# Kernel optimization log

Measured on AMD Instinct MI355X. Metric: run time of the kernel, lower is better.

## Reference

```python
import jax, jax.numpy as jnp
import numpy as np

WS = 8   # window_size
NH = 4   # num_heads
EPS = 1e-5

def _rel_pos_index(ws):
    # Static Swin relative-position index, computed with numpy (constant).
    coords = np.stack(np.meshgrid(np.arange(ws), np.arange(ws), indexing='ij'))  # [2,ws,ws]
    cf = coords.reshape(2, -1)                       # [2, N]
    rel = cf[:, :, None] - cf[:, None, :]            # [2, N, N]
    rel = rel.transpose(1, 2, 0).copy()              # [N, N, 2]
    rel[:, :, 0] += ws - 1
    rel[:, :, 1] += ws - 1
    rel[:, :, 0] *= 2 * ws - 1
    return jnp.asarray(rel.sum(-1))                  # [N, N] int

def setup_inputs() -> dict:
    key = jax.random.key(0)
    ks = jax.random.split(key, 4)
    B, C, H, W = 8, 64, 256, 256
    return {
        'x': jax.random.normal(ks[0], (B, C, H, W), jnp.float32),
        'norm_w': jnp.ones((C,), jnp.float32),
        'norm_b': jnp.zeros((C,), jnp.float32),
        'qkv_w': jax.random.normal(ks[1], (3 * C, C), jnp.float32) * 0.05,
        'proj_w': jax.random.normal(ks[2], (C, C), jnp.float32) * 0.05,
        'attn_scale': jnp.ones((1,), jnp.float32) * 0.2,
        'rpb_table': jax.random.normal(ks[3], ((2 * WS - 1) ** 2, NH), jnp.float32) * 0.02,
    }

def reference(x, norm_w, norm_b, qkv_w, proj_w, attn_scale, rpb_table):
    B, C, H, W = x.shape
    ws, nh = WS, NH
    hd = C // nh
    N = ws * ws
    nwh, nww = H // ws, W // ws  # H,W multiples of ws -> pad branch is a no-op
    # window partition: [B,C,H,W] -> [B*nwh*nww, N, C]
    xw = x.reshape(B, C, nwh, ws, nww, ws).transpose(0, 2, 4, 3, 5, 1).reshape(-1, N, C)
    # LayerNorm over channels
    mu = xw.mean(-1, keepdims=True)
    var = xw.var(-1, keepdims=True)
    xn = (xw - mu) / jnp.sqrt(var + EPS) * norm_w + norm_b
    # qkv projection (torch Linear: y = x @ W.T), split heads
    qkv = (xn @ qkv_w.T).reshape(-1, N, 3, nh, hd).transpose(2, 0, 3, 1, 4)  # [3, Wn, h, N, hd]
    q, k, v = qkv[0], qkv[1], qkv[2]
    attn = jnp.einsum('whnd,whmd->whnm', q, k) * (hd ** -0.5)  # [Wn, h, N, N]
    # gathered relative position bias
    rpi = _rel_pos_index(ws)                      # [N, N]
    bias = rpb_table[rpi].transpose(2, 0, 1)      # [h, N, N]
    attn = jax.nn.softmax(attn + bias[None], axis=-1)
    out = jnp.einsum('whnm,whmd->whnd', attn, v)  # [Wn, h, N, hd]
    out = out.transpose(0, 2, 1, 3).reshape(-1, N, C)
    out = out @ proj_w.T
    # window reverse: -> [B, C, H, W]
    out = out.reshape(B, nwh, nww, ws, ws, C).transpose(0, 5, 1, 3, 2, 4).reshape(B, C, H, W)
    return x + attn_scale * out
```

## Files before the change

### kernel.cpp

```cpp
#include <hip/hip_runtime.h>
#include <hip/hip_bf16.h>

#define WSZ 8
#define NHE 4
#define CH 64

typedef unsigned short u16;
typedef unsigned int u32;
typedef __attribute__((ext_vector_type(8))) short short8;
typedef __attribute__((ext_vector_type(4))) short short4v;
typedef __attribute__((ext_vector_type(4))) float float4v;

__device__ __forceinline__ u16 f2bf(float f) {
    __hip_bfloat16 h = __float2bfloat16(f);
    return __builtin_bit_cast(u16, h);
}
__device__ __forceinline__ int SW(int row, int col) {
    return row * 64 + (col ^ ((row & 7) << 3));
}

#define MFMA(a, b, c) __builtin_amdgcn_mfma_f32_16x16x32_bf16(a, b, c, 0, 0, 0)
#define QKSC 0.36067376022224085f

__global__ void prep(const float* __restrict__ qkvw, const float* __restrict__ projw,
                     const float* __restrict__ rpb,
                     u16* __restrict__ wq, u16* __restrict__ wp, float* __restrict__ bl)
{
    int t = blockIdx.x * 256 + threadIdx.x;
    if (t < 12288) {
        int j = t & 7, nl = (t >> 3) & 15, q = (t >> 7) & 3, kt = (t >> 9) & 1, nt = t >> 10;
        wq[t] = f2bf(qkvw[(nt * 16 + nl) * CH + kt * 32 + q * 8 + j]);
    }
    if (t < 4096) {
        int j = t & 7, nl = (t >> 3) & 15, q = (t >> 7) & 3, kt = (t >> 9) & 1, wv = t >> 10;
        wp[t] = f2bf(projw[(wv * 16 + nl) * CH + kt * 32 + q * 8 + j]);
    }
    if (t < 16384) {
        int r = t & 3, nt = (t >> 2) & 3, lane = (t >> 4) & 63, mt = (t >> 10) & 3, h = t >> 12;
        int nl = lane & 15, q = lane >> 4;
        int tokm = mt * 16 + nl, tokn = nt * 16 + q * 4 + r;
        int im = tokm >> 3, jm = tokm & 7, in_ = tokn >> 3, jn = tokn & 7;
        bl[t] = rpb[((im - in_ + 7) * 15 + (jm - jn + 7)) * NHE + h] * 1.44269504088896341f;
    }
}

__global__ __launch_bounds__(256, 5) void win_attn(
    const float* __restrict__ x, const float* __restrict__ nw, const float* __restrict__ nb,
    const u16* __restrict__ wq, const u16* __restrict__ wp,
    const float* __restrict__ ascale, const float* __restrict__ biasl,
    float* __restrict__ out, int B, int H, int W)
{
    const int HWsz = H * W;
    const int nww = W / WSZ, nwh = H / WSZ;
    const int win = (blockIdx.x & 7) * ((int)gridDim.x >> 3) + (blockIdx.x >> 3);
    const int ww = win % nww;
    const int t1 = win / nww;
    const int wh = t1 % nwh;
    const int b  = t1 / nwh;

    const int tid  = threadIdx.x;
    const int lane = tid & 63;
    const int wv   = tid >> 6;
    const int q    = lane >> 4;
    const int nl   = lane & 15;

    __shared__ alignas(16) char smem[32768];
    float* XS  = (float*)(smem);
    u16*   QO  = (u16*)(smem);
    u16*   KS  = (u16*)(smem + 8192);
    u16*   XN  = (u16*)(smem + 16384);
    u16*   VS  = (u16*)(smem + 24576);
    float* PS  = (float*)(smem + 24576);
    float* PS2 = PS + 256;

    const int rowbase = (wh * WSZ) * W + ww * WSZ;
    const float* xw = x + (size_t)b * CH * HWsz + rowbase;

    for (int e = tid; e < 1024; e += 256) {
        int c = e >> 4, r = e & 15;
        int i = r >> 1, j4 = (r & 1) * 4;
        float4v v = *(const float4v*)(xw + c * HWsz + i * W + j4);
        *(float4v*)&XS[c * 64 + i * 8 + j4] = v;
    }
    __syncthreads();

    {
        float s = 0.f, s2 = 0.f;
        #pragma unroll
        for (int ci = 0; ci < 16; ci++) {
            float v = XS[(wv * 16 + ci) * 64 + lane];
            s += v; s2 += v * v;
        }
        PS[wv * 64 + lane] = s;
        PS2[wv * 64 + lane] = s2;
    }
    __syncthreads();
    {
        float s  = PS[lane]  + PS[64 + lane]  + PS[128 + lane]  + PS[192 + lane];
        float s2 = PS2[lane] + PS2[64 + lane] + PS2[128 + lane] + PS2[192 + lane];
        float mu  = s * (1.f / 64.f);
        float var = s2 * (1.f / 64.f) - mu * mu;
        float rs  = rsqrtf(var + 1e-5f);
        #pragma unroll
        for (int ci = 0; ci < 16; ci++) {
            int c = wv * 16 + ci;
            float v = (XS[c * 64 + lane] - mu) * rs * nw[c] + nb[c];
            XN[SW(lane, c)] = f2bf(v);
        }
    }
    __syncthreads();

    {
        short8 bfrs[3][2];
        #pragma unroll
        for (int nt3 = 0; nt3 < 3; nt3++) {
            int nt = wv * 3 + nt3;
            #pragma unroll
            for (int kt = 0; kt < 2; kt++)
                bfrs[nt3][kt] = *(const short8*)&wq[((((nt * 2 + kt) * 4 + q) * 16) + nl) * 8];
        }
        short8 afr[4][2];
        #pragma unroll
        for (int mt = 0; mt < 4; mt++)
            #pragma unroll
            for (int kt = 0; kt < 2; kt++) {
                int m = mt * 16 + nl;
                int phys = (kt * 4 + q) ^ (m & 7);
                afr[mt][kt] = *(short8*)&XN[m * 64 + phys * 8];
            }
        #pragma unroll
        for (int nt3 = 0; nt3 < 3; nt3++) {
            int nt = wv * 3 + nt3;
            int which = nt >> 2;
            int chb = (nt & 3) * 16 + nl;
            #pragma unroll
            for (int mt = 0; mt < 4; mt++) {
                float4v acc = {0.f, 0.f, 0.f, 0.f};
                acc = MFMA(afr[mt][0], bfrs[nt3][0], acc);
                acc = MFMA(afr[mt][1], bfrs[nt3][1], acc);
                int tok0 = mt * 16 + q * 4;
                if (which == 0) {
                    #pragma unroll
                    for (int r = 0; r < 4; r++) QO[SW(tok0 + r, chb)] = f2bf(acc[r]);
                } else if (which == 1) {
                    #pragma unroll
                    for (int r = 0; r < 4; r++) KS[SW(tok0 + r, chb)] = f2bf(acc[r]);
                } else {
                    short4v pk;
                    pk[0] = (short)f2bf(acc[0]); pk[1] = (short)f2bf(acc[1]);
                    pk[2] = (short)f2bf(acc[2]); pk[3] = (short)f2bf(acc[3]);
                    int pt = tok0 ^ ((chb & 7) << 3);
                    *(short4v*)&VS[chb * 64 + pt] = pk;
                }
            }
        }
    }
    __syncthreads();

    {
        const int h = wv;
        u16* Pw = XN + wv * 1024;
        const short8 zero8 = {0, 0, 0, 0, 0, 0, 0, 0};
        short8 kfr[4], vfr[2];
        #pragma unroll
        for (int nt = 0; nt < 4; nt++) {
            if (q < 2) {
                int n = nt * 16 + nl;
                int phys = (h * 2 + q) ^ (n & 7);
                kfr[nt] = *(short8*)&KS[n * 64 + phys * 8];
            } else kfr[nt] = zero8;
        }
        #pragma unroll
        for (int kt = 0; kt < 2; kt++) {
            int c = h * 16 + nl;
            int phys = (kt * 4 + q) ^ (c & 7);
            vfr[kt] = *(short8*)&VS[c * 64 + phys * 8];
        }
        #pragma unroll
        for (int mt = 0; mt < 4; mt++) {
            short8 qf;
            if (q < 2) {
                int m = mt * 16 + nl;
                int phys = (h * 2 + q) ^ (m & 7);
                qf = *(short8*)&QO[m * 64 + phys * 8];
            } else qf = zero8;
            const float4v* bp = (const float4v*)(biasl + ((((h * 4 + mt) * 64) + lane) << 4));
            float4v sacc[4];
            #pragma unroll
            for (int nt = 0; nt < 4; nt++) {
                float4v z = {0.f, 0.f, 0.f, 0.f};
                sacc[nt] = MFMA(kfr[nt], qf, z);
            }
            float p[16], mx = -1e30f;
            #pragma unroll
            for (int nt = 0; nt < 4; nt++) {
                float4v blv = bp[nt];
                #pragma unroll
                for (int r = 0; r < 4; r++) {
                    float s = fmaf(sacc[nt][r], QKSC, blv[r]);
                    p[nt * 4 + r] = s;
                    mx = fmaxf(mx, s);
                }
            }
            mx = fmaxf(mx, __shfl_xor(mx, 16, 64));
            mx = fmaxf(mx, __shfl_xor(mx, 32, 64));
            float sum = 0.f;
            #pragma unroll
            for (int i = 0; i < 16; i++) {
                float e = __builtin_amdgcn_exp2f(p[i] - mx);
                p[i] = e;
                sum += e;
            }
            sum += __shfl_xor(sum, 16, 64);
            sum += __shfl_xor(sum, 32, 64);
            float inv = __builtin_amdgcn_rcpf(sum);
            #pragma unroll
            for (int nt = 0; nt < 4; nt++)
                #pragma unroll
                for (int r = 0; r < 4; r++)
                    Pw[SW(nl, nt * 16 + q * 4 + r)] = f2bf(p[nt * 4 + r] * inv);
            float4v oacc = {0.f, 0.f, 0.f, 0.f};
            #pragma unroll
            for (int kt = 0; kt < 2; kt++) {
                int phys = (kt * 4 + q) ^ (nl & 7);
                short8 pf = *(short8*)&Pw[nl * 64 + phys * 8];
                oacc = MFMA(pf, vfr[kt], oacc);
            }
            #pragma unroll
            for (int r = 0; r < 4; r++)
                QO[SW(mt * 16 + q * 4 + r, h * 16 + nl)] = f2bf(oacc[r]);
        }
    }
    __syncthreads();

    {
        const float asc = ascale[0];
        const int ch = wv * 16 + nl;
        const float* xrp = xw + (size_t)ch * HWsz;
        float4v xr[4];
        #pragma unroll
        for (int mt = 0; mt < 4; mt++) {
            int tok0 = mt * 16 + q * 4;
            xr[mt] = *(const float4v*)(xrp + (tok0 >> 3) * W + (tok0 & 7));
        }
        short8 wfr[2];
        #pragma unroll
        for (int kt = 0; kt < 2; kt++)
            wfr[kt] = *(const short8*)&wp[((((wv * 2 + kt) * 4 + q) * 16) + nl) * 8];
        float* outp = out + ((size_t)b * CH + ch) * HWsz + rowbase;
        #pragma unroll
        for (int mt = 0; mt < 4; mt++) {
            float4v yacc = {0.f, 0.f, 0.f, 0.f};
            #pragma unroll
            for (int kt = 0; kt < 2; kt++) {
                int m = mt * 16 + nl;
                int phys = (kt * 4 + q) ^ (m & 7);
                short8 of = *(short8*)&QO[m * 64 + phys * 8];
                yacc = MFMA(of, wfr[kt], yacc);
            }
            int tok0 = mt * 16 + q * 4;
            int i = tok0 >> 3, j = tok0 & 7;
            float4v y;
            y[0] = xr[mt][0] + asc * yacc[0];
            y[1] = xr[mt][1] + asc * yacc[1];
            y[2] = xr[mt][2] + asc * yacc[2];
            y[3] = xr[mt][3] + asc * yacc[3];
            *(float4v*)(outp + i * W + j) = y;
        }
    }
}

extern "C" void kernel_launch(void* const* d_in, const int* in_sizes, int n_in,
                              void* d_out, int out_size, void* d_ws, size_t ws_size,
                              hipStream_t stream) {
    const float* x     = (const float*)d_in[0];
    const float* nw    = (const float*)d_in[1];
    const float* nb    = (const float*)d_in[2];
    const float* qkvw  = (const float*)d_in[3];
    const float* projw = (const float*)d_in[4];
    const float* asc   = (const float*)d_in[5];
    const float* rpb   = (const float*)d_in[6];

    const int H = 256, W = 256;
    const int B = in_sizes[0] / (CH * H * W);
    const int nwin = B * (H / WSZ) * (W / WSZ);

    u16*   wq = (u16*)d_ws;
    u16*   wp = (u16*)((char*)d_ws + 24576);
    float* bl = (float*)((char*)d_ws + 32768);

    prep<<<64, 256, 0, stream>>>(qkvw, projw, rpb, wq, wp, bl);
    win_attn<<<nwin, 256, 0, stream>>>(x, nw, nb, wq, wp, asc, bl,
                                       (float*)d_out, B, H, W);
}
```

Measured before the change: 340.5 us.

## Load window directly into registers, drop fp32 LDS staging, shrink shared memory

Each thread now reads its 16 channel values for one token straight from global memory into registers instead of staging the whole fp32 window through LDS. LayerNorm reuses those registers and writes normalized bf16 values to LDS as packed 16-byte stores. The LDS layout is reorganized so shared memory drops from 32KB to 24KB, with an extra barrier so XN can be overlaid by QO, and the per-head P buffer moves into the V region. Launch bounds are raised to 6 blocks per CU for higher occupancy. The risks are less coalesced global loads (only 8 contiguous floats per row) and more register pressure under the tighter launch bound.

```diff
diff --git a/kernel.cpp b/kernel.cpp
--- a/kernel.cpp
+++ b/kernel.cpp
@@ -44,7 +44,7 @@
     }
 }
 
-__global__ __launch_bounds__(256, 5) void win_attn(
+__global__ __launch_bounds__(256, 6) void win_attn(
     const float* __restrict__ x, const float* __restrict__ nw, const float* __restrict__ nb,
     const u16* __restrict__ wq, const u16* __restrict__ wp,
     const float* __restrict__ ascale, const float* __restrict__ biasl,
@@ -64,94 +64,95 @@
     const int q    = lane >> 4;
     const int nl   = lane & 15;
 
-    __shared__ alignas(16) char smem[32768];
-    float* XS  = (float*)(smem);
+    __shared__ alignas(16) char smem[24576];
+    u16*   XN  = (u16*)(smem);
     u16*   QO  = (u16*)(smem);
     u16*   KS  = (u16*)(smem + 8192);
-    u16*   XN  = (u16*)(smem + 16384);
-    u16*   VS  = (u16*)(smem + 24576);
-    float* PS  = (float*)(smem + 24576);
+    u16*   VS  = (u16*)(smem + 16384);
+    float* PS  = (float*)(smem + 16384);
     float* PS2 = PS + 256;
 
     const int rowbase = (wh * WSZ) * W + ww * WSZ;
     const float* xw = x + (size_t)b * CH * HWsz + rowbase;
-
-    for (int e = tid; e < 1024; e += 256) {
-        int c = e >> 4, r = e & 15;
-        int i = r >> 1, j4 = (r & 1) * 4;
-        float4v v = *(const float4v*)(xw + c * HWsz + i * W + j4);
-        *(float4v*)&XS[c * 64 + i * 8 + j4] = v;
-    }
-    __syncthreads();
-
-    {
+    const int tokoff = (lane >> 3) * W + (lane & 7);
+
+    float xv[16];
+    {
+        const float* xc = xw + (size_t)(wv * 16) * HWsz + tokoff;
+        #pragma unroll
+        for (int ci = 0; ci < 16; ci++) xv[ci] = xc[(size_t)ci * HWsz];
         float s = 0.f, s2 = 0.f;
         #pragma unroll
-        for (int ci = 0; ci < 16; ci++) {
-            float v = XS[(wv * 16 + ci) * 64 + lane];
-            s += v; s2 += v * v;
-        }
+        for (int ci = 0; ci < 16; ci++) { s += xv[ci]; s2 += xv[ci] * xv[ci]; }
         PS[wv * 64 + lane] = s;
         PS2[wv * 64 + lane] = s2;
     }
     __syncthreads();
+
     {
         float s  = PS[lane]  + PS[64 + lane]  + PS[128 + lane]  + PS[192 + lane];
         float s2 = PS2[lane] + PS2[64 + lane] + PS2[128 + lane] + PS2[192 + lane];
         float mu  = s * (1.f / 64.f);
         float var = s2 * (1.f / 64.f) - mu * mu;
         float rs  = rsqrtf(var + 1e-5f);
+        float v[16];
         #pragma unroll
         for (int ci = 0; ci < 16; ci++) {
             int c = wv * 16 + ci;
-            float v = (XS[c * 64 + lane] - mu) * rs * nw[c] + nb[c];
-            XN[SW(lane, c)] = f2bf(v);
-        }
-    }
-    __syncthreads();
-
-    {
-        short8 bfrs[3][2];
-        #pragma unroll
-        for (int nt3 = 0; nt3 < 3; nt3++) {
-            int nt = wv * 3 + nt3;
-            #pragma unroll
-            for (int kt = 0; kt < 2; kt++)
-                bfrs[nt3][kt] = *(const short8*)&wq[((((nt * 2 + kt) * 4 + q) * 16) + nl) * 8];
-        }
-        short8 afr[4][2];
-        #pragma unroll
-        for (int mt = 0; mt < 4; mt++)
-            #pragma unroll
-            for (int kt = 0; kt < 2; kt++) {
-                int m = mt * 16 + nl;
-                int phys = (kt * 4 + q) ^ (m & 7);
-                afr[mt][kt] = *(short8*)&XN[m * 64 + phys * 8];
-            }
-        #pragma unroll
-        for (int nt3 = 0; nt3 < 3; nt3++) {
-            int nt = wv * 3 + nt3;
-            int which = nt >> 2;
-            int chb = (nt & 3) * 16 + nl;
-            #pragma unroll
-            for (int mt = 0; mt < 4; mt++) {
-                float4v acc = {0.f, 0.f, 0.f, 0.f};
-                acc = MFMA(afr[mt][0], bfrs[nt3][0], acc);
-                acc = MFMA(afr[mt][1], bfrs[nt3][1], acc);
-                int tok0 = mt * 16 + q * 4;
-                if (which == 0) {
-                    #pragma unroll
-                    for (int r = 0; r < 4; r++) QO[SW(tok0 + r, chb)] = f2bf(acc[r]);
-                } else if (which == 1) {
-                    #pragma unroll
-                    for (int r = 0; r < 4; r++) KS[SW(tok0 + r, chb)] = f2bf(acc[r]);
-                } else {
-                    short4v pk;
-                    pk[0] = (short)f2bf(acc[0]); pk[1] = (short)f2bf(acc[1]);
-                    pk[2] = (short)f2bf(acc[2]); pk[3] = (short)f2bf(acc[3]);
-                    int pt = tok0 ^ ((chb & 7) << 3);
-                    *(short4v*)&VS[chb * 64 + pt] = pk;
-                }
+            v[ci] = (xv[ci] - mu) * rs * nw[c] + nb[c];
+        }
+        #pragma unroll
+        for (int g = 0; g < 2; g++) {
+            short8 pk;
+            #pragma unroll
+            for (int j = 0; j < 8; j++) pk[j] = (short)f2bf(v[g * 8 + j]);
+            *(short8*)&XN[lane * 64 + ((wv * 16 + g * 8) ^ ((lane & 7) << 3))] = pk;
+        }
+    }
+    __syncthreads();
+
+    short8 afr[4][2];
+    #pragma unroll
+    for (int mt = 0; mt < 4; mt++)
+        #pragma unroll
+        for (int kt = 0; kt < 2; kt++) {
+            int m = mt * 16 + nl;
+            int phys = (kt * 4 + q) ^ (m & 7);
+            afr[mt][kt] = *(short8*)&XN[m * 64 + phys * 8];
+        }
+    short8 bfrs[3][2];
+    #pragma unroll
+    for (int nt3 = 0; nt3 < 3; nt3++) {
+        int nt = wv * 3 + nt3;
+        #pragma unroll
+        for (int kt = 0; kt < 2; kt++)
+            bfrs[nt3][kt] = *(const short8*)&wq[((((nt * 2 + kt) * 4 + q) * 16) + nl) * 8];
+    }
+    __syncthreads();
+
+    #pragma unroll
+    for (int nt3 = 0; nt3 < 3; nt3++) {
+        int nt = wv * 3 + nt3;
+        int which = nt >> 2;
+        int chb = (nt & 3) * 16 + nl;
+        #pragma unroll
+        for (int mt = 0; mt < 4; mt++) {
+            float4v acc = {0.f, 0.f, 0.f, 0.f};
+            acc = MFMA(afr[mt][0], bfrs[nt3][0], acc);
+            acc = MFMA(afr[mt][1], bfrs[nt3][1], acc);
+            int tok0 = mt * 16 + q * 4;
+            if (which == 0) {
+                #pragma unroll
+                for (int r = 0; r < 4; r++) QO[SW(tok0 + r, chb)] = f2bf(acc[r]);
+            } else if (which == 1) {
+                #pragma unroll
+                for (int r = 0; r < 4; r++) KS[SW(tok0 + r, chb)] = f2bf(acc[r]);
+            } else {
+                short4v pk;
+                pk[0] = (short)f2bf(acc[0]); pk[1] = (short)f2bf(acc[1]);
+                pk[2] = (short)f2bf(acc[2]); pk[3] = (short)f2bf(acc[3]);
+                int pt = tok0 ^ ((chb & 7) << 3);
+                *(short4v*)&VS[chb * 64 + pt] = pk;
             }
         }
     }
@@ -159,7 +160,6 @@
 
     {
         const int h = wv;
-        u16* Pw = XN + wv * 1024;
         const short8 zero8 = {0, 0, 0, 0, 0, 0, 0, 0};
         short8 kfr[4], vfr[2];
         #pragma unroll
@@ -176,6 +176,7 @@
             int phys = (kt * 4 + q) ^ (c & 7);
             vfr[kt] = *(short8*)&VS[c * 64 + phys * 8];
         }
+        u16* Pw = VS + h * 1024;
         #pragma unroll
         for (int mt = 0; mt < 4; mt++) {
             short8 qf;
```

New measurement: 364.5 us. 1.07x slower.

## Process four windows per block with register prefetch of next window

Applied to the files above, without the earlier changes.

Each block now handles four consecutive windows in a loop instead of one. The QKV and projection weight fragments and the scale are loaded into registers once per block. The next window's input tile is prefetched into registers while the current window's QKV, attention and projection run, hiding global load latency. In exchange the grid is four times smaller and register pressure rises, which may cut occupancy under the existing launch bounds, and an extra barrier is added per window.

```diff
diff --git a/kernel.cpp b/kernel.cpp
--- a/kernel.cpp
+++ b/kernel.cpp
@@ -4,6 +4,7 @@
 #define WSZ 8
 #define NHE 4
 #define CH 64
+#define WPB 4
 
 typedef unsigned short u16;
 typedef unsigned int u32;
@@ -52,11 +53,8 @@
 {
     const int HWsz = H * W;
     const int nww = W / WSZ, nwh = H / WSZ;
-    const int win = (blockIdx.x & 7) * ((int)gridDim.x >> 3) + (blockIdx.x >> 3);
-    const int ww = win % nww;
-    const int t1 = win / nww;
-    const int wh = t1 % nwh;
-    const int b  = t1 / nwh;
+    const int NBLK = (int)gridDim.x;
+    const int swz = (blockIdx.x & 7) * (NBLK >> 3) + ((int)blockIdx.x >> 3);
 
     const int tid  = threadIdx.x;
     const int lane = tid & 63;
@@ -73,52 +71,69 @@
     float* PS  = (float*)(smem + 24576);
     float* PS2 = PS + 256;
 
-    const int rowbase = (wh * WSZ) * W + ww * WSZ;
+    short8 bfrs[3][2];
+    #pragma unroll
+    for (int nt3 = 0; nt3 < 3; nt3++) {
+        int nt = wv * 3 + nt3;
+        #pragma unroll
+        for (int kt = 0; kt < 2; kt++)
+            bfrs[nt3][kt] = *(const short8*)&wq[((((nt * 2 + kt) * 4 + q) * 16) + nl) * 8];
+    }
+    short8 wfr[2];
+    #pragma unroll
+    for (int kt = 0; kt < 2; kt++)
+        wfr[kt] = *(const short8*)&wp[((((wv * 2 + kt) * 4 + q) * 16) + nl) * 8];
+    const float asc = ascale[0];
+
+    const int pc0 = tid >> 4;
+    const int pr  = tid & 15;
+    const int pi  = pr >> 1, pj4 = (pr & 1) * 4;
+
+    int cw = swz * WPB;
+    int rowbase, b;
+    {
+        int ww = cw % nww, t1 = cw / nww, wh = t1 % nwh; b = t1 / nwh;
+        rowbase = (wh * WSZ) * W + ww * WSZ;
+    }
     const float* xw = x + (size_t)b * CH * HWsz + rowbase;
 
-    for (int e = tid; e < 1024; e += 256) {
-        int c = e >> 4, r = e & 15;
-        int i = r >> 1, j4 = (r & 1) * 4;
-        float4v v = *(const float4v*)(xw + c * HWsz + i * W + j4);
-        *(float4v*)&XS[c * 64 + i * 8 + j4] = v;
-    }
-    __syncthreads();
-
-    {
-        float s = 0.f, s2 = 0.f;
+    float4v pre[4];
+    #pragma unroll
+    for (int it = 0; it < 4; it++)
+        pre[it] = *(const float4v*)(xw + (size_t)(pc0 + it * 16) * HWsz + pi * W + pj4);
+
+    for (int wi = 0; wi < WPB; wi++) {
         #pragma unroll
-        for (int ci = 0; ci < 16; ci++) {
-            float v = XS[(wv * 16 + ci) * 64 + lane];
-            s += v; s2 += v * v;
-        }
-        PS[wv * 64 + lane] = s;
-        PS2[wv * 64 + lane] = s2;
-    }
-    __syncthreads();
-    {
-        float s  = PS[lane]  + PS[64 + lane]  + PS[128 + lane]  + PS[192 + lane];
-        float s2 = PS2[lane] + PS2[64 + lane] + PS2[128 + lane] + PS2[192 + lane];
-        float mu  = s * (1.f / 64.f);
-        float var = s2 * (1.f / 64.f) - mu * mu;
-        float rs  = rsqrtf(var + 1e-5f);
-        #pragma unroll
-        for (int ci = 0; ci < 16; ci++) {
-            int c = wv * 16 + ci;
-            float v = (XS[c * 64 + lane] - mu) * rs * nw[c] + nb[c];
-            XN[SW(lane, c)] = f2bf(v);
-        }
-    }
-    __syncthreads();
-
-    {
-        short8 bfrs[3][2];
-        #pragma unroll
-        for (int nt3 = 0; nt3 < 3; nt3++) {
-            int nt = wv * 3 + nt3;
-            #pragma unroll
-            for (int kt = 0; kt < 2; kt++)
-                bfrs[nt3][kt] = *(const short8*)&wq[((((nt * 2 + kt) * 4 + q) * 16) + nl) * 8];
-        }
+        for (int it = 0; it < 4; it++)
+            *(float4v*)&XS[(pc0 + it * 16) * 64 + pi * 8 + pj4] = pre[it];
+        __syncthreads();
+
+        {
+            float s = 0.f, s2 = 0.f;
+            #pragma unroll
+            for (int ci = 0; ci < 16; ci++) {
+                float v = XS[(wv * 16 + ci) * 64 + lane];
+                s += v; s2 += v * v;
+            }
+            PS[wv * 64 + lane] = s;
+            PS2[wv * 64 + lane] = s2;
+        }
+        __syncthreads();
+        {
+            float s  = PS[lane]  + PS[64 + lane]  + PS[128 + lane]  + PS[192 + lane];
+            float s2 = PS2[lane] + PS2[64 + lane] + PS2[128 + lane] + PS2[192 + lane];
+            float mu  = s * (1.f / 64.f);
+            float var = s2 * (1.f / 64.f) - mu * mu;
+            float rs  = rsqrtf(var + 1e-5f);
+            #pragma unroll
+            for (int ci = 0; ci < 16; ci++) {
+                int c = wv * 16 + ci;
+                float v = (XS[c * 64 + lane] - mu) * rs * nw[c] + nb[c];
+                XN[SW(lane, c)] = f2bf(v);
+            }
+        }
+        __syncthreads();
+
         short8 afr[4][2];
         #pragma unroll
         for (int mt = 0; mt < 4; mt++)
@@ -128,6 +143,18 @@
                 int phys = (kt * 4 + q) ^ (m & 7);
                 afr[mt][kt] = *(short8*)&XN[m * 64 + phys * 8];
             }
+        int nrowbase = rowbase, nb2 = b;
+        const float* xwn = xw;
+        if (wi + 1 < WPB) {
+            int nwin2 = cw + 1;
+            int ww = nwin2 % nww, t1 = nwin2 / nww, wh = t1 % nwh; nb2 = t1 / nwh;
+            nrowbase = (wh * WSZ) * W + ww * WSZ;
+            xwn = x + (size_t)nb2 * CH * HWsz + nrowbase;
+            #pragma unroll
+            for (int it = 0; it < 4; it++)
+                pre[it] = *(const float4v*)(xwn + (size_t)(pc0 + it * 16) * HWsz + pi * W + pj4);
+        }
+
         #pragma unroll
         for (int nt3 = 0; nt3 < 3; nt3++) {
             int nt = wv * 3 + nt3;
@@ -154,119 +181,118 @@
                 }
             }
         }
-    }
-    __syncthreads();
-
-    {
-        const int h = wv;
-        u16* Pw = XN + wv * 1024;
-        const short8 zero8 = {0, 0, 0, 0, 0, 0, 0, 0};
-        short8 kfr[4], vfr[2];
-        #pragma unroll
-        for (int nt = 0; nt < 4; nt++) {
-            if (q < 2) {
-                int n = nt * 16 + nl;
-                int phys = (h * 2 + q) ^ (n & 7);
-                kfr[nt] = *(short8*)&KS[n * 64 + phys * 8];
-            } else kfr[nt] = zero8;
-        }
-        #pragma unroll
-        for (int kt = 0; kt < 2; kt++) {
-            int c = h * 16 + nl;
-            int phys = (kt * 4 + q) ^ (c & 7);
-            vfr[kt] = *(short8*)&VS[c * 64 + phys * 8];
-        }
-        #pragma unroll
-        for (int mt = 0; mt < 4; mt++) {
-            short8 qf;
-            if (q < 2) {
-                int m = mt * 16 + nl;
-                int phys = (h * 2 + q) ^ (m & 7);
-                qf = *(short8*)&QO[m * 64 + phys * 8];
-            } else qf = zero8;
-            const float4v* bp = (const float4v*)(biasl + ((((h * 4 + mt) * 64) + lane) << 4));
-            float4v sacc[4];
+        __syncthreads();
+
+        {
+            const int h = wv;
+            u16* Pw = XN + wv * 1024;
+            const short8 zero8 = {0, 0, 0, 0, 0, 0, 0, 0};
+            short8 kfr[4], vfr[2];
             #pragma unroll
             for (int nt = 0; nt < 4; nt++) {
-                float4v z = {0.f, 0.f, 0.f, 0.f};
-                sacc[nt] = MFMA(kfr[nt], qf, z);
-            }
-            float p[16], mx = -1e30f;
-            #pragma unroll
-            for (int nt = 0; nt < 4; nt++) {
-                float4v blv = bp[nt];
-                #pragma unroll
-                for (int r = 0; r < 4; r++) {
-                    float s = fmaf(sacc[nt][r], QKSC, blv[r]);
-                    p[nt * 4 + r] = s;
-                    mx = fmaxf(mx, s);
-                }
-            }
-            mx = fmaxf(mx, __shfl_xor(mx, 16, 64));
-            mx = fmaxf(mx, __shfl_xor(mx, 32, 64));
-            float sum = 0.f;
-            #pragma unroll
-            for (int i = 0; i < 16; i++) {
-                float e = __builtin_amdgcn_exp2f(p[i] - mx);
-                p[i] = e;
-                sum += e;
-            }
-            sum += __shfl_xor(sum, 16, 64);
-            sum += __shfl_xor(sum, 32, 64);
-            float inv = __builtin_amdgcn_rcpf(sum);
-            #pragma unroll
-            for (int nt = 0; nt < 4; nt++)
+                if (q < 2) {
+                    int n = nt * 16 + nl;
+                    int phys = (h * 2 + q) ^ (n & 7);
+                    kfr[nt] = *(short8*)&KS[n * 64 + phys * 8];
+                } else kfr[nt] = zero8;
+            }
+            #pragma unroll
+            for (int kt = 0; kt < 2; kt++) {
+                int c = h * 16 + nl;
+                int phys = (kt * 4 + q) ^ (c & 7);
+                vfr[kt] = *(short8*)&VS[c * 64 + phys * 8];
+            }
+            #pragma unroll
+            for (int mt = 0; mt < 4; mt++) {
+                short8 qf;
+                if (q < 2) {
+                    int m = mt * 16 + nl;
+                    int phys = (h * 2 + q) ^ (m & 7);
+                    qf = *(short8*)&QO[m * 64 + phys * 8];
+                } else qf = zero8;
+                const float4v* bp = (const float4v*)(biasl + ((((h * 4 + mt) * 64) + lane) << 4));
+                float4v sacc[4];
+                #pragma unroll
+                for (int nt = 0; nt < 4; nt++) {
+                    float4v z = {0.f, 0.f, 0.f, 0.f};
+                    sacc[nt] = MFMA(kfr[nt], qf, z);
+                }
+                float p[16], mx = -1e30f;
+                #pragma unroll
+                for (int nt = 0; nt < 4; nt++) {
+                    float4v blv = bp[nt];
+                    #pragma unroll
+                    for (int r = 0; r < 4; r++) {
+                        float s = fmaf(sacc[nt][r], QKSC, blv[r]);
+                        p[nt * 4 + r] = s;
+                        mx = fmaxf(mx, s);
+                    }
+                }
+                mx = fmaxf(mx, __shfl_xor(mx, 16, 64));
+                mx = fmaxf(mx, __shfl_xor(mx, 32, 64));
+                float sum = 0.f;
+                #pragma unroll
+                for (int i = 0; i < 16; i++) {
+                    float e = __builtin_amdgcn_exp2f(p[i] - mx);
+                    p[i] = e;
+                    sum += e;
+                }
+                sum += __shfl_xor(sum, 16, 64);
+                sum += __shfl_xor(sum, 32, 64);
+                float inv = __builtin_amdgcn_rcpf(sum);
+                #pragma unroll
+                for (int nt = 0; nt < 4; nt++)
+                    #pragma unroll
+                    for (int r = 0; r < 4; r++)
+                        Pw[SW(nl, nt * 16 + q * 4 + r)] = f2bf(p[nt * 4 + r] * inv);
+                float4v oacc = {0.f, 0.f, 0.f, 0.f};
+                #pragma unroll
+                for (int kt = 0; kt < 2; kt++) {
+                    int phys = (kt * 4 + q) ^ (nl & 7);
+                    short8 pf = *(short8*)&Pw[nl * 64 + phys * 8];
+                    oacc = MFMA(pf, vfr[kt], oacc);
+                }
                 #pragma unroll
                 for (int r = 0; r < 4; r++)
-                    Pw[SW(nl, nt * 16 + q * 4 + r)] = f2bf(p[nt * 4 + r] * inv);
-            float4v oacc = {0.f, 0.f, 0.f, 0.f};
-            #pragma unroll
-            for (int kt = 0; kt < 2; kt++) {
-                int phys = (kt * 4 + q) ^ (nl & 7);
-                short8 pf = *(short8*)&Pw[nl * 64 + phys * 8];
-                oacc = MFMA(pf, vfr[kt], oacc);
-            }
-            #pragma unroll
-            for (int r = 0; r < 4; r++)
-                QO[SW(mt * 16 + q * 4 + r, h * 16 + nl)] = f2bf(oacc[r]);
-        }
-    }
-    __syncthreads();
-
-    {
-        const float asc = ascale[0];
-        const int ch = wv * 16 + nl;
-        const float* xrp = xw + (size_t)ch * HWsz;
-        float4v xr[4];
-        #pragma unroll
-        for (int mt = 0; mt < 4; mt++) {
-            int tok0 = mt * 16 + q * 4;
-            xr[mt] = *(const float4v*)(xrp + (tok0 >> 3) * W + (tok0 & 7));
-        }
-        short8 wfr[2];
-        #pragma unroll
-        for (int kt = 0; kt < 2; kt++)
-            wfr[kt] = *(const short8*)&wp[((((wv * 2 + kt) * 4 + q) * 16) + nl) * 8];
-        float* outp = out + ((size_t)b * CH + ch) * HWsz + rowbase;
-        #pragma unroll
-        for (int mt = 0; mt < 4; mt++) {
-            float4v yacc = {0.f, 0.f, 0.f, 0.f};
-            #pragma unroll
-            for (int kt = 0; kt < 2; kt++) {
-                int m = mt * 16 + nl;
-                int phys = (kt * 4 + q) ^ (m & 7);
-                short8 of = *(short8*)&QO[m * 64 + phys * 8];
-                yacc = MFMA(of, wfr[kt], yacc);
-            }
-            int tok0 = mt * 16 + q * 4;
-            int i = tok0 >> 3, j = tok0 & 7;
-            float4v y;
-            y[0] = xr[mt][0] + asc * yacc[0];
-            y[1] = xr[mt][1] + asc * yacc[1];
-            y[2] = xr[mt][2] + asc * yacc[2];
-            y[3] = xr[mt][3] + asc * yacc[3];
-            *(float4v*)(outp + i * W + j) = y;
-        }
+                    QO[SW(mt * 16 + q * 4 + r, h * 16 + nl)] = f2bf(oacc[r]);
+            }
+        }
+        __syncthreads();
+
+        {
+            const int ch = wv * 16 + nl;
+            const float* xrp = xw + (size_t)ch * HWsz;
+            float4v xr[4];
+            #pragma unroll
+            for (int mt = 0; mt < 4; mt++) {
+                int tok0 = mt * 16 + q * 4;
+                xr[mt] = *(const float4v*)(xrp + (tok0 >> 3) * W + (tok0 & 7));
+            }
+            float* outp = out + ((size_t)b * CH + ch) * HWsz + rowbase;
+            #pragma unroll
+            for (int mt = 0; mt < 4; mt++) {
+                float4v yacc = {0.f, 0.f, 0.f, 0.f};
+                #pragma unroll
+                for (int kt = 0; kt < 2; kt++) {
+                    int m = mt * 16 + nl;
+                    int phys = (kt * 4 + q) ^ (m & 7);
+                    short8 of = *(short8*)&QO[m * 64 + phys * 8];
+                    yacc = MFMA(of, wfr[kt], yacc);
+                }
+                int tok0 = mt * 16 + q * 4;
+                int i = tok0 >> 3, j = tok0 & 7;
+                float4v y;
+                y[0] = xr[mt][0] + asc * yacc[0];
+                y[1] = xr[mt][1] + asc * yacc[1];
+                y[2] = xr[mt][2] + asc * yacc[2];
+                y[3] = xr[mt][3] + asc * yacc[3];
+                *(float4v*)(outp + i * W + j) = y;
+            }
+        }
+        __syncthreads();
+
+        cw++;
+        rowbase = nrowbase; b = nb2; xw = xwn;
     }
 }
 
@@ -284,12 +310,13 @@
     const int H = 256, W = 256;
     const int B = in_sizes[0] / (CH * H * W);
     const int nwin = B * (H / WSZ) * (W / WSZ);
+    const int nblk = nwin / WPB;
 
     u16*   wq = (u16*)d_ws;
     u16*   wp = (u16*)((char*)d_ws + 24576);
     float* bl = (float*)((char*)d_ws + 32768);
 
     prep<<<64, 256, 0, stream>>>(qkvw, projw, rpb, wq, wp, bl);
-    win_attn<<<nwin, 256, 0, stream>>>(x, nw, nb, wq, wp, asc, bl,
+    win_attn<<<nblk, 256, 0, stream>>>(x, nw, nb, wq, wp, asc, bl,
                                        (float*)d_out, B, H, W);
 }
```

Result: slower. 1.328 ms (+290.0%).
